# Performance work log

Hardware: AMD Instinct MI355X
Metric: run time of the kernel (lower is better)

## Reference

```python
import jax, jax.numpy as jnp
import numpy as np

M, N, K = 1024, 11008, 4096


def _unpack_i2u(Bp):
    """Unpack 2-bit unsigned weights per decode_i2u_to_i8s interleave.

    Bp: [N, K//4] int8 storage. Within each group of 4 bytes (16 elements),
    output element at position 4*i + j = (byte_j >> (2*i)) & 3.
    Returns [N, K] int8 with values in {0,1,2,3}.
    """
    Bu = jax.lax.bitcast_convert_type(Bp, jnp.uint8)  # [N, K//4]
    n, kc = Bu.shape
    Bg = Bu.reshape(n, kc // 4, 1, 4)                 # [N, G, 1, j]
    shifts = (jnp.arange(4, dtype=jnp.uint8) * jnp.uint8(2)).reshape(1, 1, 4, 1)
    vals = (Bg >> shifts) & jnp.uint8(3)              # [N, G, i, j]
    return vals.reshape(n, kc * 4).astype(jnp.int8)   # [N, K]


def setup_inputs() -> dict:
    key = jax.random.key(0)
    k1, k2 = jax.random.split(key)
    A = jax.random.randint(k1, (M, K), -128, 128, dtype=jnp.int8)
    B = jax.random.randint(k2, (N, K // 4), -128, 128, dtype=jnp.int8)
    return {"A": A, "B": B}


def reference(A, B):
    W = _unpack_i2u(B)  # [N, K] int8
    C = jax.lax.dot_general(
        A, W,
        dimension_numbers=(((1,), (1,)), ((), ())),
        preferred_element_type=jnp.int32,
    )  # [M, N] int32
    return C
```

## Files before the change

kernel.cpp:

```cpp
#include <hip/hip_runtime.h>
#include <stdint.h>


#define MM 1024
#define NN 11008
#define KK 4096
#define KSTEPS 64
#define MTILES (MM / 128)
#define NTILES (NN / 128)

using i32x4  = __attribute__((ext_vector_type(4))) int;
using i32x16 = __attribute__((ext_vector_type(16))) int;

__device__ __forceinline__ int pack4(i32x4 v) {
    return (int)(((uint32_t)v[0] & 0xFFu) | (((uint32_t)v[1] & 0xFFu) << 8)
               | (((uint32_t)v[2] & 0xFFu) << 16) | (((uint32_t)v[3] & 0xFFu) << 24));
}

__global__ __launch_bounds__(256) void prep_A(const int* __restrict__ src,
                                              uint8_t* __restrict__ dst) {
    const int g = blockIdx.x * 256 + threadIdx.x;
    const int kstep = g >> 12;
    const int rem   = g & 4095;
    const int mtile = rem >> 9;
    const int c     = rem & 511;
    const int row32 = (c >> 7) & 3, kk2 = (c >> 6) & 1;
    const int lane  = c & 63;
    const int row   = mtile * 128 + row32 * 32 + (lane & 31);
    const int kbyte = kstep * 64 + kk2 * 32 + (lane >> 5) * 16;
    const i32x4* s4 = (const i32x4*)(src + (size_t)row * KK + kbyte);
    i32x4 o;
#pragma unroll
    for (int q = 0; q < 4; ++q) o[q] = pack4(s4[q]);
    *(i32x4*)(dst + (size_t)g * 16) = o;
}

__global__ __launch_bounds__(256) void prep_B(const int* __restrict__ src,
                                              uint8_t* __restrict__ dst) {
    const int t = blockIdx.x * 256 + threadIdx.x;
    const int lane = t & 63;
    const int wc   = (t >> 6) & 1;
    const int rem  = t >> 7;
    const int ntile = rem % NTILES;
    const int kstep = rem / NTILES;
    const int l31 = lane & 31, h = lane >> 5;
    i32x4 o;
#pragma unroll
    for (int q = 0; q < 4; ++q) {
        const int ni = q >> 1, kk2 = q & 1;
        const int n  = ntile * 128 + wc * 64 + ni * 32 + l31;
        const i32x4 v = *(const i32x4*)(src + (size_t)n * (KK / 4) + kstep * 16 + kk2 * 8 + h * 4);
        o[q] = pack4(v);
    }
    *(i32x4*)(dst + (size_t)t * 16) = o;
}

__global__ __launch_bounds__(256, 3) void bitnet_gemm(const uint8_t* __restrict__ A2,
                                                      const uint8_t* __restrict__ B3,
                                                      int* __restrict__ C) {
    const int t    = threadIdx.x;
    const int lane = t & 63, wave = t >> 6;
    const int wr   = wave >> 1, wc = wave & 1;
    const int l31  = lane & 31, h = lane >> 5;
    const int by   = blockIdx.y, bx = blockIdx.x;

    const size_t strideA = (size_t)MTILES * 8192;
    const size_t strideB = (size_t)NTILES * 2048;

    const uint8_t* pa[4];
#pragma unroll
    for (int s = 0; s < 4; ++s) {
        const int mi = s >> 1, kk2 = s & 1;
        pa[s] = A2 + (size_t)by * 8192 + ((wr * 2 + mi) * 2 + kk2) * 1024 + lane * 16;
    }
    const uint8_t* pb = B3 + (size_t)bx * 2048 + wc * 1024 + lane * 16;

    i32x16 acc[2][2] = {};
    i32x4 a0[4], a1[4], p0, p1;

    auto LOAD = [&](i32x4 (&a)[4], i32x4& p, int ks) {
#pragma unroll
        for (int s = 0; s < 4; ++s)
            a[s] = *(const i32x4*)(pa[s] + (size_t)ks * strideA);
        p = *(const i32x4*)(pb + (size_t)ks * strideB);
    };

    auto COMPUTE = [&](const i32x4 (&a)[4], const i32x4& p) {
#pragma unroll
        for (int kk2 = 0; kk2 < 2; ++kk2) {
            const uint32_t q0 = (uint32_t)p[kk2];
            const uint32_t q1 = (uint32_t)p[2 + kk2];
            i32x4 b0, b1;
#pragma unroll
            for (int i = 0; i < 4; ++i) {
                b0[i] = (int)((q0 >> (2 * i)) & 0x03030303u);
                b1[i] = (int)((q1 >> (2 * i)) & 0x03030303u);
            }
            acc[0][0] = __builtin_amdgcn_mfma_i32_32x32x32_i8(a[0 * 2 + kk2], b0, acc[0][0], 0, 0, 0);
            acc[0][1] = __builtin_amdgcn_mfma_i32_32x32x32_i8(a[0 * 2 + kk2], b1, acc[0][1], 0, 0, 0);
            acc[1][0] = __builtin_amdgcn_mfma_i32_32x32x32_i8(a[1 * 2 + kk2], b0, acc[1][0], 0, 0, 0);
            acc[1][1] = __builtin_amdgcn_mfma_i32_32x32x32_i8(a[1 * 2 + kk2], b1, acc[1][1], 0, 0, 0);
        }
    };

    LOAD(a0, p0, 0);
    LOAD(a1, p1, 1);

#pragma unroll 1
    for (int ks = 0; ks < KSTEPS - 2; ks += 2) {
        COMPUTE(a0, p0);
        LOAD(a0, p0, ks + 2);
        COMPUTE(a1, p1);
        LOAD(a1, p1, ks + 3);
    }
    COMPUTE(a0, p0);
    COMPUTE(a1, p1);

    const int brow = by * 128, bcol = bx * 128;
#pragma unroll
    for (int mi = 0; mi < 2; ++mi)
#pragma unroll
        for (int ni = 0; ni < 2; ++ni) {
            const int colg = bcol + wc * 64 + ni * 32 + l31;
#pragma unroll
            for (int r = 0; r < 16; ++r) {
                const int rowin = (r & 3) + 8 * (r >> 2) + 4 * h;
                const int rowg  = brow + wr * 64 + mi * 32 + rowin;
                C[(size_t)rowg * NN + colg] = acc[mi][ni][r];
            }
        }
}

extern "C" void kernel_launch(void* const* d_in, const int* in_sizes, int n_in,
                              void* d_out, int out_size, void* d_ws, size_t ws_size,
                              hipStream_t stream) {
    const int* A32 = (const int*)d_in[0];
    const int* B32 = (const int*)d_in[1];
    int* C = (int*)d_out;

    uint8_t* A2 = (uint8_t*)d_ws;
    uint8_t* B3 = A2 + (size_t)MM * KK;

    prep_A<<<dim3((MM * KK / 16) / 256), dim3(256), 0, stream>>>(A32, A2);
    prep_B<<<dim3((NN * 64) / 256), dim3(256), 0, stream>>>(B32, B3);
    bitnet_gemm<<<dim3(NTILES, MTILES), dim3(256), 0, stream>>>(A2, B3, C);
}
```

Baseline: 73.53 us.

## Stage A tiles through LDS with a deep async pipeline and swizzle blocks

The two prep kernels merge into one launch, and the B prep is rewritten so each thread reads a contiguous weight row chunk. The GEMM now stages A tiles into a 6-slot LDS ring with global_load_lds, keeping 5 stages in flight. Because a block's four waves share the staged A tile, each wave no longer fetches its own copy from global memory. A remapped 1D grid groups blocks that share B columns for better L2 reuse. The cost is 48KB of LDS per block, which may limit occupancy to 3 blocks per CU, plus a barrier on every k-step.

After: 64.43 us. 12.4% less time.

```diff
diff --git a/kernel.cpp b/kernel.cpp
--- a/kernel.cpp
+++ b/kernel.cpp
@@ -6,8 +6,11 @@
 #define NN 11008
 #define KK 4096
 #define KSTEPS 64
-#define MTILES (MM / 128)
-#define NTILES (NN / 128)
+#define MTILES 8
+#define NTILES 86
+#define NBLOCKS (MTILES * NTILES)
+#define STRIDE_A ((size_t)MTILES * 8192)
+#define STRIDE_B ((size_t)NTILES * 2048)
 
 using i32x4  = __attribute__((ext_vector_type(4))) int;
 using i32x16 = __attribute__((ext_vector_type(16))) int;
@@ -17,106 +20,128 @@
                | (((uint32_t)v[2] & 0xFFu) << 16) | (((uint32_t)v[3] & 0xFFu) << 24));
 }
 
-__global__ __launch_bounds__(256) void prep_A(const int* __restrict__ src,
-                                              uint8_t* __restrict__ dst) {
-    const int g = blockIdx.x * 256 + threadIdx.x;
-    const int kstep = g >> 12;
-    const int rem   = g & 4095;
-    const int mtile = rem >> 9;
-    const int c     = rem & 511;
-    const int row32 = (c >> 7) & 3, kk2 = (c >> 6) & 1;
-    const int lane  = c & 63;
-    const int row   = mtile * 128 + row32 * 32 + (lane & 31);
-    const int kbyte = kstep * 64 + kk2 * 32 + (lane >> 5) * 16;
-    const i32x4* s4 = (const i32x4*)(src + (size_t)row * KK + kbyte);
-    i32x4 o;
+__global__ __launch_bounds__(256) void prep_AB(const int* __restrict__ Asrc,
+                                               const int* __restrict__ Bsrc,
+                                               uint8_t* __restrict__ A2,
+                                               uint8_t* __restrict__ B3) {
+    if (blockIdx.x < 1024) {
+        const int g = blockIdx.x * 256 + threadIdx.x;
+        const int kstep = g >> 12;
+        const int rem   = g & 4095;
+        const int mtile = rem >> 9;
+        const int c     = rem & 511;
+        const int row32 = (c >> 7) & 3, kk2 = (c >> 6) & 1;
+        const int lane  = c & 63;
+        const int row   = mtile * 128 + row32 * 32 + (lane & 31);
+        const int kbyte = kstep * 64 + kk2 * 32 + (lane >> 5) * 16;
+        const i32x4* s4 = (const i32x4*)(Asrc + (size_t)row * KK + kbyte);
+        i32x4 o;
 #pragma unroll
-    for (int q = 0; q < 4; ++q) o[q] = pack4(s4[q]);
-    *(i32x4*)(dst + (size_t)g * 16) = o;
+        for (int q = 0; q < 4; ++q) o[q] = pack4(s4[q]);
+        *(i32x4*)(A2 + (size_t)g * 16) = o;
+    } else {
+        const int t = (blockIdx.x - 1024) * 256 + threadIdx.x;
+        const int n = t >> 6, kstep = t & 63;
+        const int ntile = n >> 7, wc = (n >> 6) & 1, ni = (n >> 5) & 1, l31 = n & 31;
+        const i32x4* s4 = (const i32x4*)(Bsrc + (size_t)n * (KK / 4) + kstep * 16);
+        int w[4];
+#pragma unroll
+        for (int j = 0; j < 4; ++j) w[j] = pack4(s4[j]);
+        uint8_t* base = B3 + ((size_t)kstep * NTILES + ntile) * 2048 + wc * 1024;
+        *(int2*)(base + l31 * 16 + ni * 8)        = make_int2(w[0], w[2]);
+        *(int2*)(base + (l31 + 32) * 16 + ni * 8) = make_int2(w[1], w[3]);
+    }
 }
 
-__global__ __launch_bounds__(256) void prep_B(const int* __restrict__ src,
-                                              uint8_t* __restrict__ dst) {
-    const int t = blockIdx.x * 256 + threadIdx.x;
-    const int lane = t & 63;
-    const int wc   = (t >> 6) & 1;
-    const int rem  = t >> 7;
-    const int ntile = rem % NTILES;
-    const int kstep = rem / NTILES;
-    const int l31 = lane & 31, h = lane >> 5;
-    i32x4 o;
-#pragma unroll
-    for (int q = 0; q < 4; ++q) {
-        const int ni = q >> 1, kk2 = q & 1;
-        const int n  = ntile * 128 + wc * 64 + ni * 32 + l31;
-        const i32x4 v = *(const i32x4*)(src + (size_t)n * (KK / 4) + kstep * 16 + kk2 * 8 + h * 4);
-        o[q] = pack4(v);
-    }
-    *(i32x4*)(dst + (size_t)t * 16) = o;
-}
+#define GLOAD_LDS16(g, l) __builtin_amdgcn_global_load_lds(                    \
+        (const __attribute__((address_space(1))) uint32_t*)(g),                \
+        (__attribute__((address_space(3))) uint32_t*)(l), 16, 0, 0)
+
+#define MFMA_I8 __builtin_amdgcn_mfma_i32_32x32x32_i8
+
+#define STAGE(KS, SLOT) do {                                                   \
+    const uint8_t* at_ = gA + (size_t)(KS) * STRIDE_A;                         \
+    GLOAD_LDS16(at_,        &As[SLOT][wave * 1024]);                           \
+    GLOAD_LDS16(at_ + 4096, &As[SLOT][4096 + wave * 1024]);                    \
+} while (0)
+
+#define BLOAD(BI, KS) bb[BI] = *(const i32x4*)(gB + (size_t)(KS) * STRIDE_B)
+
+#define COMP(SLOT, BI) do {                                                    \
+    _Pragma("unroll")                                                          \
+    for (int kk2_ = 0; kk2_ < 2; ++kk2_) {                                     \
+        i32x4 a0_ = *(const i32x4*)(&As[SLOT][(wr * 2 + 0) * 2048 + kk2_ * 1024 + lane * 16]); \
+        i32x4 a1_ = *(const i32x4*)(&As[SLOT][(wr * 2 + 1) * 2048 + kk2_ * 1024 + lane * 16]); \
+        const uint32_t q0_ = (uint32_t)bb[BI][0 * 2 + kk2_];                   \
+        const uint32_t q1_ = (uint32_t)bb[BI][1 * 2 + kk2_];                   \
+        i32x4 b0_, b1_;                                                        \
+        _Pragma("unroll")                                                      \
+        for (int i_ = 0; i_ < 4; ++i_) {                                       \
+            b0_[i_] = (int)((q0_ >> (2 * i_)) & 0x03030303u);                  \
+            b1_[i_] = (int)((q1_ >> (2 * i_)) & 0x03030303u);                  \
+        }                                                                      \
+        acc[0][0] = MFMA_I8(a0_, b0_, acc[0][0], 0, 0, 0);                     \
+        acc[0][1] = MFMA_I8(a0_, b1_, acc[0][1], 0, 0, 0);                     \
+        acc[1][0] = MFMA_I8(a1_, b0_, acc[1][0], 0, 0, 0);                     \
+        acc[1][1] = MFMA_I8(a1_, b1_, acc[1][1], 0, 0, 0);                     \
+    }                                                                          \
+} while (0)
+
+#define ITER(T, SLOT, BCUR, BNXT, NW, DOSTAGE, DOB) do {                       \
+    asm volatile("s_waitcnt vmcnt(" #NW ")" ::: "memory");                     \
+    __builtin_amdgcn_s_barrier();                                              \
+    asm volatile("" ::: "memory");                                             \
+    __builtin_amdgcn_sched_barrier(0);                                         \
+    if (DOSTAGE) STAGE((T) + 5, ((SLOT) + 5) % 6);                             \
+    if (DOB) BLOAD(BNXT, (T) + 2);                                             \
+    COMP(SLOT, BCUR);                                                          \
+} while (0)
 
 __global__ __launch_bounds__(256, 3) void bitnet_gemm(const uint8_t* __restrict__ A2,
                                                       const uint8_t* __restrict__ B3,
                                                       int* __restrict__ C) {
-    const int t    = threadIdx.x;
-    const int lane = t & 63, wave = t >> 6;
+    const int tid  = threadIdx.x;
+    const int lane = tid & 63, wave = tid >> 6;
     const int wr   = wave >> 1, wc = wave & 1;
     const int l31  = lane & 31, h = lane >> 5;
-    const int by   = blockIdx.y, bx = blockIdx.x;
 
-    const size_t strideA = (size_t)MTILES * 8192;
-    const size_t strideB = (size_t)NTILES * 2048;
+    const int bid = blockIdx.x;
+    const int l   = (bid & 7) * (NBLOCKS / 8) + (bid >> 3);
+    const int bm  = l & 7;
+    const int bn  = l >> 3;
 
-    const uint8_t* pa[4];
-#pragma unroll
-    for (int s = 0; s < 4; ++s) {
-        const int mi = s >> 1, kk2 = s & 1;
-        pa[s] = A2 + (size_t)by * 8192 + ((wr * 2 + mi) * 2 + kk2) * 1024 + lane * 16;
-    }
-    const uint8_t* pb = B3 + (size_t)bx * 2048 + wc * 1024 + lane * 16;
+    __shared__ __align__(16) uint8_t As[6][8192];
+
+    const uint8_t* gA = A2 + (size_t)bm * 8192 + tid * 16;
+    const uint8_t* gB = B3 + (size_t)bn * 2048 + wc * 1024 + lane * 16;
 
     i32x16 acc[2][2] = {};
-    i32x4 a0[4], a1[4], p0, p1;
+    i32x4 bb[3];
 
-    auto LOAD = [&](i32x4 (&a)[4], i32x4& p, int ks) {
-#pragma unroll
-        for (int s = 0; s < 4; ++s)
-            a[s] = *(const i32x4*)(pa[s] + (size_t)ks * strideA);
-        p = *(const i32x4*)(pb + (size_t)ks * strideB);
-    };
-
-    auto COMPUTE = [&](const i32x4 (&a)[4], const i32x4& p) {
-#pragma unroll
-        for (int kk2 = 0; kk2 < 2; ++kk2) {
-            const uint32_t q0 = (uint32_t)p[kk2];
-            const uint32_t q1 = (uint32_t)p[2 + kk2];
-            i32x4 b0, b1;
-#pragma unroll
-            for (int i = 0; i < 4; ++i) {
-                b0[i] = (int)((q0 >> (2 * i)) & 0x03030303u);
-                b1[i] = (int)((q1 >> (2 * i)) & 0x03030303u);
-            }
-            acc[0][0] = __builtin_amdgcn_mfma_i32_32x32x32_i8(a[0 * 2 + kk2], b0, acc[0][0], 0, 0, 0);
-            acc[0][1] = __builtin_amdgcn_mfma_i32_32x32x32_i8(a[0 * 2 + kk2], b1, acc[0][1], 0, 0, 0);
-            acc[1][0] = __builtin_amdgcn_mfma_i32_32x32x32_i8(a[1 * 2 + kk2], b0, acc[1][0], 0, 0, 0);
-            acc[1][1] = __builtin_amdgcn_mfma_i32_32x32x32_i8(a[1 * 2 + kk2], b1, acc[1][1], 0, 0, 0);
-        }
-    };
-
-    LOAD(a0, p0, 0);
-    LOAD(a1, p1, 1);
+    STAGE(0, 0); STAGE(1, 1); STAGE(2, 2); STAGE(3, 3); STAGE(4, 4);
+    BLOAD(0, 0); BLOAD(1, 1);
 
 #pragma unroll 1
-    for (int ks = 0; ks < KSTEPS - 2; ks += 2) {
-        COMPUTE(a0, p0);
-        LOAD(a0, p0, ks + 2);
-        COMPUTE(a1, p1);
-        LOAD(a1, p1, ks + 3);
+    for (int t = 0; t < 54; t += 6) {
+        ITER(t + 0, 0, 0, 2, 10, true, true);
+        ITER(t + 1, 1, 1, 0, 10, true, true);
+        ITER(t + 2, 2, 2, 1, 10, true, true);
+        ITER(t + 3, 3, 0, 2, 10, true, true);
+        ITER(t + 4, 4, 1, 0, 10, true, true);
+        ITER(t + 5, 5, 2, 1, 10, true, true);
     }
-    COMPUTE(a0, p0);
-    COMPUTE(a1, p1);
+    ITER(54, 0, 0, 2, 10, true,  true);
+    ITER(55, 1, 1, 0, 10, true,  true);
+    ITER(56, 2, 2, 1, 10, true,  true);
+    ITER(57, 3, 0, 2, 10, true,  true);
+    ITER(58, 4, 1, 0, 10, true,  true);
+    ITER(59, 5, 2, 1, 10, false, true);
+    ITER(60, 0, 0, 2, 10, false, true);
+    ITER(61, 1, 1, 0, 8,  false, true);
+    ITER(62, 2, 2, 1, 6,  false, false);
+    ITER(63, 3, 0, 2, 4,  false, false);
 
-    const int brow = by * 128, bcol = bx * 128;
+    const int brow = bm * 128, bcol = bn * 128;
 #pragma unroll
     for (int mi = 0; mi < 2; ++mi)
 #pragma unroll
@@ -141,7 +166,6 @@
     uint8_t* A2 = (uint8_t*)d_ws;
     uint8_t* B3 = A2 + (size_t)MM * KK;
 
-    prep_A<<<dim3((MM * KK / 16) / 256), dim3(256), 0, stream>>>(A32, A2);
-    prep_B<<<dim3((NN * 64) / 256), dim3(256), 0, stream>>>(B32, B3);
-    bitnet_gemm<<<dim3(NTILES, MTILES), dim3(256), 0, stream>>>(A2, B3, C);
+    prep_AB<<<dim3(1024 + 2752), dim3(256), 0, stream>>>(A32, B32, A2, B3);
+    bitnet_gemm<<<dim3(NBLOCKS), dim3(256), 0, stream>>>(A2, B3, C);
 }
```
